# Kernel tuning notes

Measured on AMD Instinct MI355X. Metric: run time of the kernel, lower is better.

Reference implementation:

```python
import jax, jax.numpy as jnp
import numpy as np

N, E, D = 100000, 400000, 128

def setup_inputs() -> dict:
    key = jax.random.key(0)
    k1, k2, k3, k4, k5 = jax.random.split(key, 5)
    x = jax.random.normal(k1, (N, D), dtype=jnp.float32)
    e = jax.random.normal(k2, (E, D), dtype=jnp.float32)
    # torch nn.Linear(3D, D, bias=False) weight is [D, 3D]; we store W = weight.T -> [3D, D]
    W = jax.random.normal(k3, (3 * D, D), dtype=jnp.float32) * (1.0 / np.sqrt(3 * D))
    src_idx = jax.random.randint(k4, (E,), 0, N, dtype=jnp.int64)
    dst_idx = jax.random.randint(k5, (E,), 0, N, dtype=jnp.int64)
    return {"x": x, "e": e, "W": W, "src_idx": src_idx, "dst_idx": dst_idx}

def reference(x, e, W, src_idx, dst_idx):
    # message = Linear(concat([src_feat, tgt_feat, role_feat], -1))
    # Split W into the three d-blocks so we never materialize the [E, 3D] concat:
    # concat([a,b,c]) @ W == a@W1 + b@W2 + c@W3  (exactly the same math)
    d = x.shape[-1]
    W_src, W_dst, W_e = W[:d], W[d:2 * d], W[2 * d:]
    m = x[src_idx] @ W_src + x[dst_idx] @ W_dst + e @ W_e  # [E, D]
    return m
```

## Files before the change

### kernel.cpp

```cpp
#include <hip/hip_runtime.h>
#include <hip/hip_bf16.h>

typedef __attribute__((ext_vector_type(8))) short bf16x8;
typedef __attribute__((ext_vector_type(4))) float f32x4;

#define D128 128
#define IMG_SHORTS 16384
#define XB_OFF 65536
#define NBLK 256
#define WSH (3 * IMG_SHORTS)
#define RBS 4096

__device__ __forceinline__ short f2bf(float f) {
    union { float f; unsigned u; } v; v.f = f;
    unsigned r = (v.u + 0x7FFFu + ((v.u >> 16) & 1u)) >> 16;
    return (short)r;
}

__device__ __forceinline__ short f2bf_h(float f) {
    __hip_bfloat16 h = __float2bfloat16(f);
    short s;
    __builtin_memcpy(&s, &h, sizeof(short));
    return s;
}

__device__ __forceinline__ bf16x8 pack8(f32x4 a, f32x4 b) {
    bf16x8 r;
    r[0] = f2bf_h(a[0]); r[1] = f2bf_h(a[1]); r[2] = f2bf_h(a[2]); r[3] = f2bf_h(a[3]);
    r[4] = f2bf_h(b[0]); r[5] = f2bf_h(b[1]); r[6] = f2bf_h(b[2]); r[7] = f2bf_h(b[3]);
    return r;
}

__device__ __forceinline__ void gload_lds16(const short* g, short* l) {
    __builtin_amdgcn_global_load_lds(
        (const __attribute__((address_space(1))) unsigned int*)(const void*)g,
        (__attribute__((address_space(3))) unsigned int*)(void*)l, 16, 0, 0);
}

__global__ __launch_bounds__(256) void wt_kernel(const float* __restrict__ W,
                                                 short* __restrict__ Wimg) {
    const int c    = blockIdx.x >> 3;
    const int frag = (blockIdx.x & 7) * 4 + (threadIdx.x >> 6);
    const int lane = threadIdx.x & 63;
    const int mt = frag >> 2, ks = frag & 3;
    const int m  = mt * 16 + (lane & 15);
    const int k0 = ks * 32 + (lane >> 4) * 8;
    bf16x8 v;
#pragma unroll
    for (int j = 0; j < 8; ++j)
        v[j] = f2bf(W[(size_t)(c * 128 + k0 + j) * D128 + m]);
    *reinterpret_cast<bf16x8*>(
        &Wimg[((size_t)c * 32 + frag) * 64 * 8 + (size_t)lane * 8]) = v;
}

__global__ __launch_bounds__(256) void xb_kernel(const float* __restrict__ x,
                                                 short* __restrict__ xb) {
    const size_t i = ((size_t)blockIdx.x * 256 + threadIdx.x) * 8;
    f32x4 v0 = reinterpret_cast<const f32x4*>(x + i)[0];
    f32x4 v1 = reinterpret_cast<const f32x4*>(x + i)[1];
    *reinterpret_cast<bf16x8*>(xb + i) = pack8(v0, v1);
}

__global__ __launch_bounds__(512, 2) void fused_kernel(
        const short* __restrict__ xb,
        const float* __restrict__ e,
        const short* __restrict__ Wimg,
        const int*  __restrict__ src_idx,
        const int*  __restrict__ dst_idx,
        float* __restrict__ out,
        int E, int ntiles)
{
    __shared__ short lds[WSH + 8 * RBS];

    const int tid  = threadIdx.x;
    const int lane = tid & 63;
    const int w    = tid >> 6;
    const int r    = lane >> 2;
    const int q    = lane & 3;
    const int sx   = (r >> 1) & 3;
    const int fr   = lane & 15;
    const int lhi  = lane >> 4;
    const int rb_off = (fr * 4 + (lhi ^ ((fr >> 1) & 3))) * 8;

    short* RB = &lds[WSH + w * RBS];
    short* BB = RB + 2048;

    const int per = ntiles >> 8;
    const int rem = ntiles & 255;
    const int b   = blockIdx.x;
    const int t0  = b * per + (b < rem ? b : rem);
    const int t1  = t0 + per + (b < rem ? 1 : 0);

#pragma unroll
    for (int jj = 0; jj < 12; ++jj) {
        int unit = jj * 512 + tid;
        gload_lds16(Wimg + (size_t)unit * 8, &lds[unit * 8]);
    }
    asm volatile("" ::: "memory");
    asm volatile("s_waitcnt vmcnt(0)" ::: "memory");
    __builtin_amdgcn_s_barrier();

    int rp = t0 * 128 + w * 16 + r;
    int si = src_idx[rp];
    int di = dst_idx[rp];
    bf16x8 sl[4];
#pragma unroll
    for (int ks = 0; ks < 4; ++ks)
        sl[ks] = *reinterpret_cast<const bf16x8*>(
            xb + (size_t)si * D128 + ks * 32 + (q ^ sx) * 8);
    f32x4 ev[8];
    {
        const float* pe = e + (size_t)(t0 * 128 + w * 16 + fr) * D128;
#pragma unroll
        for (int ks = 0; ks < 4; ++ks) {
            ev[2 * ks]     = reinterpret_cast<const f32x4*>(pe + ks * 32 + lhi * 8)[0];
            ev[2 * ks + 1] = reinterpret_cast<const f32x4*>(pe + ks * 32 + lhi * 8)[1];
        }
    }
    int rpn = (t0 + 1) * 128 + w * 16 + r;
    if (rpn >= E) rpn = E - 1;
    int sn = src_idx[rpn];
    int dn = dst_idx[rpn];
    asm volatile("" ::: "memory");

    for (int t = t0; t < t1; ++t) {
        const int rn = t * 128 + w * 16 + fr;

#pragma unroll
        for (int ks = 0; ks < 4; ++ks)
            *reinterpret_cast<bf16x8*>(&RB[ks * 512 + lane * 8]) = sl[ks];
        asm volatile("" ::: "memory");

        bf16x8 dl[4];
#pragma unroll
        for (int ks = 0; ks < 4; ++ks)
            dl[ks] = *reinterpret_cast<const bf16x8*>(
                xb + (size_t)di * D128 + ks * 32 + (q ^ sx) * 8);
#pragma unroll
        for (int ks = 0; ks < 4; ++ks)
            sl[ks] = *reinterpret_cast<const bf16x8*>(
                xb + (size_t)sn * D128 + ks * 32 + (q ^ sx) * 8);
        asm volatile("" ::: "memory");

        f32x4 acc[8];
#pragma unroll
        for (int mt = 0; mt < 8; ++mt) acc[mt] = (f32x4){0.f, 0.f, 0.f, 0.f};

#pragma unroll
        for (int ks = 0; ks < 4; ++ks) {
            bf16x8 bfr = *reinterpret_cast<const bf16x8*>(&RB[ks * 512 + rb_off]);
#pragma unroll
            for (int mt = 0; mt < 8; ++mt) {
                bf16x8 a = *reinterpret_cast<const bf16x8*>(
                    &lds[((0 * 32 + mt * 4 + ks) * 64 + lane) * 8]);
                acc[mt] = __builtin_amdgcn_mfma_f32_16x16x32_bf16(a, bfr, acc[mt], 0, 0, 0);
            }
        }
        asm volatile("" ::: "memory");

#pragma unroll
        for (int ks = 0; ks < 4; ++ks)
            *reinterpret_cast<bf16x8*>(&BB[ks * 512 + lane * 8]) = dl[ks];
        asm volatile("" ::: "memory");

#pragma unroll
        for (int ks = 0; ks < 4; ++ks) {
            bf16x8 bfr = *reinterpret_cast<const bf16x8*>(&BB[ks * 512 + rb_off]);
#pragma unroll
            for (int mt = 0; mt < 8; ++mt) {
                bf16x8 a = *reinterpret_cast<const bf16x8*>(
                    &lds[((1 * 32 + mt * 4 + ks) * 64 + lane) * 8]);
                acc[mt] = __builtin_amdgcn_mfma_f32_16x16x32_bf16(a, bfr, acc[mt], 0, 0, 0);
            }
        }

#pragma unroll
        for (int ks = 0; ks < 4; ++ks) {
            bf16x8 be = pack8(ev[2 * ks], ev[2 * ks + 1]);
#pragma unroll
            for (int mt = 0; mt < 8; ++mt) {
                bf16x8 a = *reinterpret_cast<const bf16x8*>(
                    &lds[((2 * 32 + mt * 4 + ks) * 64 + lane) * 8]);
                acc[mt] = __builtin_amdgcn_mfma_f32_16x16x32_bf16(a, be, acc[mt], 0, 0, 0);
            }
        }

        float* po = out + (size_t)rn * D128 + lhi * 4;
#pragma unroll
        for (int mt = 0; mt < 8; ++mt)
            *reinterpret_cast<f32x4*>(po + mt * 16) = acc[mt];
        asm volatile("" ::: "memory");

        di = dn;
        {
            int ern = (t + 1) * 128 + w * 16 + fr;
            if (ern >= E) ern = E - 1;
            const float* pe = e + (size_t)ern * D128;
#pragma unroll
            for (int ks = 0; ks < 4; ++ks) {
                ev[2 * ks]     = reinterpret_cast<const f32x4*>(pe + ks * 32 + lhi * 8)[0];
                ev[2 * ks + 1] = reinterpret_cast<const f32x4*>(pe + ks * 32 + lhi * 8)[1];
            }
        }
        int rp2 = (t + 2) * 128 + w * 16 + r;
        if (rp2 >= E) rp2 = E - 1;
        sn = src_idx[rp2];
        dn = dst_idx[rp2];
        asm volatile("" ::: "memory");
    }
}

extern "C" void kernel_launch(void* const* d_in, const int* in_sizes, int n_in,
                              void* d_out, int out_size, void* d_ws, size_t ws_size,
                              hipStream_t stream) {
    const float* x = (const float*)d_in[0];
    const float* e = (const float*)d_in[1];
    const float* W = (const float*)d_in[2];
    const int* src = (const int*)d_in[3];
    const int* dst = (const int*)d_in[4];
    float* out = (float*)d_out;

    short* Wimg = (short*)d_ws;
    short* xb   = (short*)d_ws + XB_OFF;

    const int N = in_sizes[0] / D128;
    const int E = in_sizes[3];
    const int ntiles = E / 128;

    wt_kernel<<<24, 256, 0, stream>>>(W, Wimg);
    xb_kernel<<<(N * D128) / (256 * 8), 256, 0, stream>>>(x, xb);
    fused_kernel<<<NBLK, 512, 0, stream>>>(xb, e, Wimg, src, dst, out, E, ntiles);
}
```

Baseline: 133.8 us.

## Split output columns across two blocks and use bpermute instead of LDS staging

Each edge tile is now processed by two blocks, each computing half of the output columns with half of the weight image in LDS, which lowers LDS use and allows more resident blocks. The gathered src/dst rows are rearranged into MFMA B-fragment order with ds_bpermute rather than being written to and reread from LDS. The trade-off is that both halves re-gather the same x rows and reread the fp32 edge features, which roughly doubles the input read traffic.

```diff
diff --git a/kernel.cpp b/kernel.cpp
--- a/kernel.cpp
+++ b/kernel.cpp
@@ -3,13 +3,12 @@
 
 typedef __attribute__((ext_vector_type(8))) short bf16x8;
 typedef __attribute__((ext_vector_type(4))) float f32x4;
+typedef __attribute__((ext_vector_type(4))) int i32x4;
 
 #define D128 128
 #define IMG_SHORTS 16384
 #define XB_OFF 65536
-#define NBLK 256
-#define WSH (3 * IMG_SHORTS)
-#define RBS 4096
+#define WSH_HALF 24576
 
 __device__ __forceinline__ short f2bf(float f) {
     union { float f; unsigned u; } v; v.f = f;
@@ -29,6 +28,15 @@
     r[0] = f2bf_h(a[0]); r[1] = f2bf_h(a[1]); r[2] = f2bf_h(a[2]); r[3] = f2bf_h(a[3]);
     r[4] = f2bf_h(b[0]); r[5] = f2bf_h(b[1]); r[6] = f2bf_h(b[2]); r[7] = f2bf_h(b[3]);
     return r;
+}
+
+__device__ __forceinline__ bf16x8 bperm8(int addr, bf16x8 v) {
+    i32x4 iv = __builtin_bit_cast(i32x4, v);
+    i32x4 ov;
+#pragma unroll
+    for (int i = 0; i < 4; ++i)
+        ov[i] = __builtin_amdgcn_ds_bpermute(addr, iv[i]);
+    return __builtin_bit_cast(bf16x8, ov);
 }
 
 __device__ __forceinline__ void gload_lds16(const short* g, short* l) {
@@ -61,7 +69,7 @@
     *reinterpret_cast<bf16x8*>(xb + i) = pack8(v0, v1);
 }
 
-__global__ __launch_bounds__(512, 2) void fused_kernel(
+__global__ __launch_bounds__(512, 4) void fused_kernel(
         const short* __restrict__ xb,
         const float* __restrict__ e,
         const short* __restrict__ Wimg,
@@ -70,44 +78,45 @@
         float* __restrict__ out,
         int E, int ntiles)
 {
-    __shared__ short lds[WSH + 8 * RBS];
+    __shared__ short lds[WSH_HALF];
 
     const int tid  = threadIdx.x;
     const int lane = tid & 63;
     const int w    = tid >> 6;
     const int r    = lane >> 2;
     const int q    = lane & 3;
-    const int sx   = (r >> 1) & 3;
     const int fr   = lane & 15;
     const int lhi  = lane >> 4;
-    const int rb_off = (fr * 4 + (lhi ^ ((fr >> 1) & 3))) * 8;
-
-    short* RB = &lds[WSH + w * RBS];
-    short* BB = RB + 2048;
+    const int bp   = ((lane & 15) * 4 + (lane >> 4)) * 4;
+
+    const int h  = blockIdx.x >> 8;
+    const int rb = blockIdx.x & 255;
 
     const int per = ntiles >> 8;
     const int rem = ntiles & 255;
-    const int b   = blockIdx.x;
-    const int t0  = b * per + (b < rem ? b : rem);
-    const int t1  = t0 + per + (b < rem ? 1 : 0);
-
-#pragma unroll
-    for (int jj = 0; jj < 12; ++jj) {
-        int unit = jj * 512 + tid;
-        gload_lds16(Wimg + (size_t)unit * 8, &lds[unit * 8]);
+    const int t0  = rb * per + (rb < rem ? rb : rem);
+    const int t1  = t0 + per + (rb < rem ? 1 : 0);
+
+#pragma unroll
+    for (int jj = 0; jj < 6; ++jj) {
+        int u    = jj * 512 + tid;
+        int c    = u >> 10;
+        int rm   = u & 1023;
+        gload_lds16(Wimg + ((size_t)(c * 32 + h * 16)) * 512 + (size_t)rm * 8,
+                    &lds[u * 8]);
     }
+    int rp = t0 * 128 + w * 16 + r;
+    int si = src_idx[rp];
+    int di = dst_idx[rp];
     asm volatile("" ::: "memory");
     asm volatile("s_waitcnt vmcnt(0)" ::: "memory");
     __builtin_amdgcn_s_barrier();
 
-    int rp = t0 * 128 + w * 16 + r;
-    int si = src_idx[rp];
-    int di = dst_idx[rp];
     bf16x8 sl[4];
 #pragma unroll
     for (int ks = 0; ks < 4; ++ks)
         sl[ks] = *reinterpret_cast<const bf16x8*>(
-            xb + (size_t)si * D128 + ks * 32 + (q ^ sx) * 8);
+            xb + (size_t)si * D128 + ks * 32 + q * 8);
     f32x4 ev[8];
     {
         const float* pe = e + (size_t)(t0 * 128 + w * 16 + fr) * D128;
@@ -126,50 +135,39 @@
     for (int t = t0; t < t1; ++t) {
         const int rn = t * 128 + w * 16 + fr;
 
-#pragma unroll
-        for (int ks = 0; ks < 4; ++ks)
-            *reinterpret_cast<bf16x8*>(&RB[ks * 512 + lane * 8]) = sl[ks];
-        asm volatile("" ::: "memory");
-
-        bf16x8 dl[4];
+        bf16x8 dl[4], nl[4];
 #pragma unroll
         for (int ks = 0; ks < 4; ++ks)
             dl[ks] = *reinterpret_cast<const bf16x8*>(
-                xb + (size_t)di * D128 + ks * 32 + (q ^ sx) * 8);
+                xb + (size_t)di * D128 + ks * 32 + q * 8);
 #pragma unroll
         for (int ks = 0; ks < 4; ++ks)
-            sl[ks] = *reinterpret_cast<const bf16x8*>(
-                xb + (size_t)sn * D128 + ks * 32 + (q ^ sx) * 8);
+            nl[ks] = *reinterpret_cast<const bf16x8*>(
+                xb + (size_t)sn * D128 + ks * 32 + q * 8);
         asm volatile("" ::: "memory");
 
-        f32x4 acc[8];
-#pragma unroll
-        for (int mt = 0; mt < 8; ++mt) acc[mt] = (f32x4){0.f, 0.f, 0.f, 0.f};
-
-#pragma unroll
-        for (int ks = 0; ks < 4; ++ks) {
-            bf16x8 bfr = *reinterpret_cast<const bf16x8*>(&RB[ks * 512 + rb_off]);
-#pragma unroll
-            for (int mt = 0; mt < 8; ++mt) {
+        f32x4 acc[4];
+#pragma unroll
+        for (int mt = 0; mt < 4; ++mt) acc[mt] = (f32x4){0.f, 0.f, 0.f, 0.f};
+
+#pragma unroll
+        for (int ks = 0; ks < 4; ++ks) {
+            bf16x8 bfr = bperm8(bp, sl[ks]);
+#pragma unroll
+            for (int mt = 0; mt < 4; ++mt) {
                 bf16x8 a = *reinterpret_cast<const bf16x8*>(
-                    &lds[((0 * 32 + mt * 4 + ks) * 64 + lane) * 8]);
+                    &lds[((0 * 16 + mt * 4 + ks) * 64 + lane) * 8]);
                 acc[mt] = __builtin_amdgcn_mfma_f32_16x16x32_bf16(a, bfr, acc[mt], 0, 0, 0);
             }
         }
-        asm volatile("" ::: "memory");
-
-#pragma unroll
-        for (int ks = 0; ks < 4; ++ks)
-            *reinterpret_cast<bf16x8*>(&BB[ks * 512 + lane * 8]) = dl[ks];
-        asm volatile("" ::: "memory");
-
-#pragma unroll
-        for (int ks = 0; ks < 4; ++ks) {
-            bf16x8 bfr = *reinterpret_cast<const bf16x8*>(&BB[ks * 512 + rb_off]);
-#pragma unroll
-            for (int mt = 0; mt < 8; ++mt) {
+
+#pragma unroll
+        for (int ks = 0; ks < 4; ++ks) {
+            bf16x8 bfr = bperm8(bp, dl[ks]);
+#pragma unroll
+            for (int mt = 0; mt < 4; ++mt) {
                 bf16x8 a = *reinterpret_cast<const bf16x8*>(
-                    &lds[((1 * 32 + mt * 4 + ks) * 64 + lane) * 8]);
+                    &lds[((1 * 16 + mt * 4 + ks) * 64 + lane) * 8]);
                 acc[mt] = __builtin_amdgcn_mfma_f32_16x16x32_bf16(a, bfr, acc[mt], 0, 0, 0);
             }
         }
@@ -178,20 +176,21 @@
         for (int ks = 0; ks < 4; ++ks) {
             bf16x8 be = pack8(ev[2 * ks], ev[2 * ks + 1]);
 #pragma unroll
-            for (int mt = 0; mt < 8; ++mt) {
+            for (int mt = 0; mt < 4; ++mt) {
                 bf16x8 a = *reinterpret_cast<const bf16x8*>(
-                    &lds[((2 * 32 + mt * 4 + ks) * 64 + lane) * 8]);
+                    &lds[((2 * 16 + mt * 4 + ks) * 64 + lane) * 8]);
                 acc[mt] = __builtin_amdgcn_mfma_f32_16x16x32_bf16(a, be, acc[mt], 0, 0, 0);
             }
         }
 
-        float* po = out + (size_t)rn * D128 + lhi * 4;
-#pragma unroll
-        for (int mt = 0; mt < 8; ++mt)
+        float* po = out + (size_t)rn * D128 + h * 64 + lhi * 4;
+#pragma unroll
+        for (int mt = 0; mt < 4; ++mt)
             *reinterpret_cast<f32x4*>(po + mt * 16) = acc[mt];
         asm volatile("" ::: "memory");
 
-        di = dn;
+        si = sn; di = dn;
+        sl[0] = nl[0]; sl[1] = nl[1]; sl[2] = nl[2]; sl[3] = nl[3];
         {
             int ern = (t + 1) * 128 + w * 16 + fr;
             if (ern >= E) ern = E - 1;
@@ -229,5 +228,5 @@
 
     wt_kernel<<<24, 256, 0, stream>>>(W, Wimg);
     xb_kernel<<<(N * D128) / (256 * 8), 256, 0, stream>>>(x, xb);
-    fused_kernel<<<NBLK, 512, 0, stream>>>(xb, e, Wimg, src, dst, out, E, ntiles);
-}
+    fused_kernel<<<512, 512, 0, stream>>>(xb, e, Wimg, src, dst, out, E, ntiles);
+}
```

New measurement: 183.7 us. 1.37x slower.
